# Performance work log

Hardware: AMD Instinct MI355X
Metric: run time of the kernel (lower is better)

Reference implementation:

```python
import jax, jax.numpy as jnp
import numpy as np

N = 50000      # nodes
E = 800000     # edges
R = 8          # relations
DIN, DH, DOUT = 128, 128, 64
EPS = 1e-5     # BatchNorm eps


def setup_inputs() -> dict:
    key = jax.random.key(0)
    ks = jax.random.split(key, 24)
    w = lambda k, shape, fan_in: jax.random.normal(k, shape, jnp.float32) / np.sqrt(fan_in)
    x = jax.random.normal(ks[0], (N, DIN), jnp.float32)
    edge_index = jax.random.randint(ks[1], (2, E), 0, N, dtype=jnp.int64)
    edge_type = jax.random.randint(ks[2], (E,), 0, R, dtype=jnp.int64)
    return {
        "x": x, "edge_index": edge_index, "edge_type": edge_type,
        # layer 1: RGCN(DIN->DH) + BN
        "W1": w(ks[3], (R, DIN, DH), DIN), "Wr1": w(ks[4], (DIN, DH), DIN), "b1": jnp.zeros((DH,), jnp.float32),
        "g1": jnp.ones((DH,), jnp.float32), "be1": jnp.zeros((DH,), jnp.float32),
        "rm1": 0.1 * jax.random.normal(ks[5], (DH,), jnp.float32),
        "rv1": jax.random.uniform(ks[6], (DH,), jnp.float32, 0.5, 1.5),
        # layer 2: RGCN(DH->DH) + BN
        "W2": w(ks[7], (R, DH, DH), DH), "Wr2": w(ks[8], (DH, DH), DH), "b2": jnp.zeros((DH,), jnp.float32),
        "g2": jnp.ones((DH,), jnp.float32), "be2": jnp.zeros((DH,), jnp.float32),
        "rm2": 0.1 * jax.random.normal(ks[9], (DH,), jnp.float32),
        "rv2": jax.random.uniform(ks[10], (DH,), jnp.float32, 0.5, 1.5),
        # layer 3: RGCN(DH->DOUT)
        "W3": w(ks[11], (R, DH, DOUT), DH), "Wr3": w(ks[12], (DH, DOUT), DH), "b3": jnp.zeros((DOUT,), jnp.float32),
    }


def rgcn_layer(x, W, Wroot, b, src, dst, et):
    # PyG RGCNConv: per-relation linear transform, per-relation MEAN aggregation
    # over incoming edges, plus root transform and bias.
    nR, nN, H = W.shape[0], x.shape[0], W.shape[2]
    h = jnp.einsum('nd,rdh->rnh', x, W)          # [R,N,H] per-relation transform
    msg = h[et, src]                             # [E,H] gather per edge
    seg = dst * nR + et                          # segment key = (node, relation)
    sums = jax.ops.segment_sum(msg, seg, num_segments=nN * nR)
    cnt = jax.ops.segment_sum(jnp.ones((seg.shape[0],), x.dtype), seg, num_segments=nN * nR)
    mean = sums / jnp.maximum(cnt, 1.0)[:, None]
    agg = mean.reshape(nN, nR, H).sum(axis=1)    # sum over relations
    return agg + x @ Wroot + b


def batchnorm(x, g, b, rm, rv):
    # eval-mode BatchNorm1d with running stats
    return (x - rm) * jax.lax.rsqrt(rv + EPS) * g + b


def reference(x, edge_index, edge_type,
              W1, Wr1, b1, g1, be1, rm1, rv1,
              W2, Wr2, b2, g2, be2, rm2, rv2,
              W3, Wr3, b3):
    src, dst = edge_index[0], edge_index[1]
    h = rgcn_layer(x, W1, Wr1, b1, src, dst, edge_type)
    h = jax.nn.relu(batchnorm(h, g1, be1, rm1, rv1))  # dropout: eval mode = identity
    h = rgcn_layer(h, W2, Wr2, b2, src, dst, edge_type)
    h = jax.nn.relu(batchnorm(h, g2, be2, rm2, rv2))
    h = rgcn_layer(h, W3, Wr3, b3, src, dst, edge_type)
    return jax.nn.sigmoid(h)
```

## Files before the change

kernel.cpp:

```cpp
#include <hip/hip_runtime.h>

typedef _Float16 f16;
typedef __attribute__((ext_vector_type(8))) _Float16 half8;
typedef __attribute__((ext_vector_type(2))) _Float16 half2v;
typedef __attribute__((ext_vector_type(4))) float float4v;

#define NNODES 50000
#define NEDGES 800000
#define NREL 8
#define NRSEG (NNODES * NREL)
#define KDIM 1152
#define CAP 16
#define CAPQ (CAP / 4)
#define NT64 ((NNODES + 63) / 64)

__global__ void bucket_fill(const int* __restrict__ src, const int* __restrict__ dst,
                            const int* __restrict__ et, int* __restrict__ cnt,
                            int* __restrict__ esrc) {
    int e = blockIdx.x * blockDim.x + threadIdx.x;
    if (e < NEDGES) {
        int s = dst[e] * NREL + et[e];
        int p = atomicAdd(&cnt[s], 1);
        if (p < CAP) esrc[s * CAP + p] = src[e];
    }
}

__global__ void setup_misc(const float* __restrict__ x, f16* __restrict__ x16,
                           const float* __restrict__ W1, const float* __restrict__ Wr1,
                           const float* __restrict__ W2, const float* __restrict__ Wr2,
                           const float* __restrict__ W3, const float* __restrict__ Wr3,
                           f16* __restrict__ Bt, int* __restrict__ cnt) {
    int t = blockIdx.x * blockDim.x + threadIdx.x;
    if (t < NNODES * 64) {
        float2 v = ((const float2*)x)[t];
        half2v o = {(f16)v.x, (f16)v.y};
        ((half2v*)x16)[t] = o;
        return;
    }
    int idx = t - NNODES * 64;
    if (idx < 320 * KDIM) {
        int hg = idx / KDIM, k = idx - hg * KDIM;
        const float *W, *Wr;
        int h, H;
        if (hg < 128)      { W = W1; Wr = Wr1; h = hg;       H = 128; }
        else if (hg < 256) { W = W2; Wr = Wr2; h = hg - 128; H = 128; }
        else               { W = W3; Wr = Wr3; h = hg - 256; H = 64;  }
        float v = (k < 1024) ? W[(size_t)k * H + h] : Wr[(size_t)(k - 1024) * H + h];
        Bt[idx] = (f16)v;
        return;
    }
    int z = idx - 320 * KDIM;
    if (z < NRSEG / 4) ((int4*)cnt)[z] = (int4){0, 0, 0, 0};
}

template <int H, int HB, int MODE>
__global__ __launch_bounds__(256, 4) void fused_layer(
    const f16* __restrict__ act, const f16* __restrict__ Bt,
    const int* __restrict__ cnt, const int* __restrict__ esrc,
    const float* __restrict__ bias, const float* __restrict__ g,
    const float* __restrict__ be, const float* __restrict__ rm,
    const float* __restrict__ rv, f16* __restrict__ hout, float* __restrict__ fout) {
    constexpr int NT = HB / 16;
    __shared__ f16 Ws[HB][128];
    const int tid = threadIdx.x;
    const int wave = tid >> 6, lane = tid & 63;
    const int l15 = lane & 15, quad = lane >> 4;
    const int m0 = blockIdx.x * 64 + wave * 16;
    const int nh = blockIdx.y;
    int node = m0 + l15;
    node = node < NNODES ? node : NNODES - 1;

    int4 cq0 = ((const int4*)cnt)[node * 2];
    int4 cq1 = ((const int4*)cnt)[node * 2 + 1];
    int cnts[8] = {cq0.x, cq0.y, cq0.z, cq0.w, cq1.x, cq1.y, cq1.z, cq1.w};
    const int4* bq_base = (const int4*)esrc + (size_t)node * NREL * CAPQ;

    float4v acc[NT];
#pragma unroll
    for (int j = 0; j < NT; ++j) acc[j] = (float4v){0.f, 0.f, 0.f, 0.f};

    int4 qp0 = bq_base[0];
    int4 qp1 = bq_base[CAPQ];

#pragma unroll
    for (int r = 0; r < 9; ++r) {
        __syncthreads();
#pragma unroll
        for (int i = 0; i < NT; ++i) {
            int G = i * 256 + tid;
            int row = G >> 4, gg = G & 15;
            half8 v = *(const half8*)(Bt + (size_t)(nh * HB + row) * KDIM +
                                      r * 128 + gg * 8);
            *(half8*)&Ws[row][((gg ^ (row & 7))) * 8] = v;
        }
        half8 ch[4];
#pragma unroll
        for (int t = 0; t < 4; ++t) ch[t] = (half8)(f16)0.f;
        if (r < 8) {
            int truelen = cnts[r];
            int len = truelen < CAP ? truelen : CAP;
            f16 invh = (f16)(truelen > 1 ? 1.f / (float)truelen : 1.f);
            const int4* bq = bq_base + r * CAPQ;
            int4 q0 = qp0;
            qp0 = qp1;
            if (r < 6) qp1 = bq_base[(r + 2) * CAPQ];
            for (int j4 = 0; j4 < (len + 3) >> 2; ++j4) {
                int4 q = (j4 == 0) ? q0 : bq[j4];
                int ids[4] = {q.x, q.y, q.z, q.w};
                int base = j4 * 4;
#pragma unroll
                for (int t = 0; t < 4; ++t) {
                    if (base + t < len) {
                        const half8* rp = (const half8*)(act + (size_t)ids[t] * 128 + quad * 8);
                        half8 v0 = rp[0], v1 = rp[4], v2 = rp[8], v3 = rp[12];
                        ch[0] += v0;
                        ch[1] += v1;
                        ch[2] += v2;
                        ch[3] += v3;
                    }
                }
            }
            half8 sv;
#pragma unroll
            for (int u = 0; u < 8; ++u) sv[u] = invh;
#pragma unroll
            for (int t = 0; t < 4; ++t) ch[t] *= sv;
        } else {
#pragma unroll
            for (int ks = 0; ks < 4; ++ks)
                ch[ks] = *(const half8*)(act + (size_t)node * 128 + ks * 32 + quad * 8);
        }
        __syncthreads();
#pragma unroll
        for (int ks = 0; ks < 4; ++ks) {
#pragma unroll
            for (int nt = 0; nt < NT; ++nt) {
                int row = nt * 16 + l15;
                half8 bf = *(const half8*)&Ws[row][(((ks * 4 + quad) ^ (row & 7))) * 8];
                acc[nt] = __builtin_amdgcn_mfma_f32_16x16x32_f16(ch[ks], bf, acc[nt], 0, 0, 0);
            }
        }
    }

#pragma unroll
    for (int nt = 0; nt < NT; ++nt) {
        int col = nh * HB + nt * 16 + l15;
        float alpha, beta;
        if (MODE == 0) {
            float sc = g[col] * rsqrtf(rv[col] + 1e-5f);
            alpha = sc;
            beta = (bias[col] - rm[col]) * sc + be[col];
        } else {
            alpha = 1.f;
            beta = bias[col];
        }
#pragma unroll
        for (int rg = 0; rg < 4; ++rg) {
            int row = m0 + quad * 4 + rg;
            if (row < NNODES) {
                float v = fmaf(acc[nt][rg], alpha, beta);
                if (MODE == 0) {
                    hout[(size_t)row * H + col] = (f16)fmaxf(v, 0.f);
                } else {
                    fout[(size_t)row * H + col] = 1.f / (1.f + __expf(-v));
                }
            }
        }
    }
}

extern "C" void kernel_launch(void* const* d_in, const int* in_sizes, int n_in,
                              void* d_out, int out_size, void* d_ws, size_t ws_size,
                              hipStream_t stream) {
    (void)in_sizes; (void)n_in; (void)out_size; (void)ws_size;
    const float* x   = (const float*)d_in[0];
    const int* ei    = (const int*)d_in[1];
    const int* et    = (const int*)d_in[2];
    const float* W1  = (const float*)d_in[3];
    const float* Wr1 = (const float*)d_in[4];
    const float* b1  = (const float*)d_in[5];
    const float* g1  = (const float*)d_in[6];
    const float* be1 = (const float*)d_in[7];
    const float* rm1 = (const float*)d_in[8];
    const float* rv1 = (const float*)d_in[9];
    const float* W2  = (const float*)d_in[10];
    const float* Wr2 = (const float*)d_in[11];
    const float* b2  = (const float*)d_in[12];
    const float* g2  = (const float*)d_in[13];
    const float* be2 = (const float*)d_in[14];
    const float* rm2 = (const float*)d_in[15];
    const float* rv2 = (const float*)d_in[16];
    const float* W3  = (const float*)d_in[17];
    const float* Wr3 = (const float*)d_in[18];
    const float* b3  = (const float*)d_in[19];
    const int* src = ei;
    const int* dst = ei + NEDGES;
    float* out = (float*)d_out;

    char* ws = (char*)d_ws;
    size_t off = 0;
    auto alloc = [&](size_t bytes) -> void* {
        off = (off + 255) & ~(size_t)255;
        void* p = ws + off;
        off += bytes;
        return p;
    };
    int* cnt  = (int*)alloc((size_t)NRSEG * 4);
    int* esrc = (int*)alloc((size_t)NRSEG * CAP * 4);
    f16* x16  = (f16*)alloc((size_t)NNODES * 128 * 2);
    f16* ha   = (f16*)alloc((size_t)NNODES * 128 * 2);
    f16* hb   = (f16*)alloc((size_t)NNODES * 128 * 2);
    f16* Bt   = (f16*)alloc((size_t)320 * KDIM * 2);

    const int SETUP_T = NNODES * 64 + 320 * KDIM + NRSEG / 4;
    setup_misc<<<(SETUP_T + 255) / 256, 256, 0, stream>>>(
        x, x16, W1, Wr1, W2, Wr2, W3, Wr3, Bt, cnt);
    bucket_fill<<<(NEDGES + 255) / 256, 256, 0, stream>>>(src, dst, et, cnt, esrc);

    fused_layer<128, 64, 0><<<dim3(NT64, 2), 256, 0, stream>>>(x16, Bt, cnt, esrc,
                                                               b1, g1, be1, rm1, rv1, ha, nullptr);
    fused_layer<128, 64, 0><<<dim3(NT64, 2), 256, 0, stream>>>(ha, Bt + (size_t)128 * KDIM, cnt, esrc,
                                                               b2, g2, be2, rm2, rv2, hb, nullptr);
    fused_layer<64, 32, 1><<<dim3(NT64, 2), 256, 0, stream>>>(hb, Bt + (size_t)256 * KDIM, cnt, esrc,
                                                              b3, nullptr, nullptr, nullptr, nullptr,
                                                              nullptr, out);
}
```

Baseline: 464.1 us.

## Sort per-segment source buckets and compute full output width per block

Adds a bucket_sort kernel that sorts each (node, relation) bucket of source indices, so the later gathers read neighbour rows in ascending address order and get better cache locality. The fused layers now launch one block per 64-node tile covering the whole output width instead of splitting it across two blocks, which removes the duplicated gather and aggregation work. The costs are an extra kernel launch with a sort pass over all 400K segments, and heavier per-block work that may raise register pressure and cut occupancy.

```diff
diff --git a/kernel.cpp b/kernel.cpp
--- a/kernel.cpp
+++ b/kernel.cpp
@@ -13,6 +13,7 @@
 #define CAP 16
 #define CAPQ (CAP / 4)
 #define NT64 ((NNODES + 63) / 64)
+#define IMAX 0x7fffffff
 
 __global__ void bucket_fill(const int* __restrict__ src, const int* __restrict__ dst,
                             const int* __restrict__ et, int* __restrict__ cnt,
@@ -22,6 +23,48 @@
         int s = dst[e] * NREL + et[e];
         int p = atomicAdd(&cnt[s], 1);
         if (p < CAP) esrc[s * CAP + p] = src[e];
+    }
+}
+
+__device__ __forceinline__ void ce(int& a, int& b) {
+    int lo = min(a, b), hi = max(a, b);
+    a = lo; b = hi;
+}
+__global__ void bucket_sort(const int* __restrict__ cnt, int* __restrict__ esrc) {
+    int s = blockIdx.x * blockDim.x + threadIdx.x;
+    if (s >= NRSEG) return;
+    int len = cnt[s];
+    len = len < CAP ? len : CAP;
+    if (len < 2) return;
+    int* b = esrc + (size_t)s * CAP;
+    if (len <= 4) {
+        int4 q = *(int4*)b;
+        int v0 = q.x, v1 = len > 1 ? q.y : IMAX;
+        int v2 = len > 2 ? q.z : IMAX, v3 = len > 3 ? q.w : IMAX;
+        ce(v0, v1); ce(v2, v3); ce(v0, v2); ce(v1, v3); ce(v1, v2);
+        *(int4*)b = (int4){v0, v1, v2, v3};
+    } else if (len <= 8) {
+        int4 qa = ((int4*)b)[0], qb = ((int4*)b)[1];
+        int v0 = qa.x, v1 = qa.y, v2 = qa.z, v3 = qa.w;
+        int v4 = qb.x, v5 = len > 5 ? qb.y : IMAX;
+        int v6 = len > 6 ? qb.z : IMAX, v7 = len > 7 ? qb.w : IMAX;
+        ce(v0, v1); ce(v2, v3); ce(v4, v5); ce(v6, v7);
+        ce(v0, v2); ce(v1, v3); ce(v4, v6); ce(v5, v7);
+        ce(v1, v2); ce(v5, v6);
+        ce(v0, v4); ce(v1, v5); ce(v2, v6); ce(v3, v7);
+        ce(v2, v4); ce(v3, v5);
+        ce(v1, v2); ce(v3, v4); ce(v5, v6);
+        ((int4*)b)[0] = (int4){v0, v1, v2, v3};
+        ((int4*)b)[1] = (int4){v4, v5, v6, v7};
+    } else {
+        int v[CAP];
+        for (int i = 0; i < len; ++i) v[i] = b[i];
+        for (int i = 1; i < len; ++i) {
+            int key = v[i], j = i - 1;
+            while (j >= 0 && v[j] > key) { v[j + 1] = v[j]; --j; }
+            v[j + 1] = key;
+        }
+        for (int i = 0; i < len; ++i) b[i] = v[i];
     }
 }
 
@@ -216,12 +259,13 @@
     setup_misc<<<(SETUP_T + 255) / 256, 256, 0, stream>>>(
         x, x16, W1, Wr1, W2, Wr2, W3, Wr3, Bt, cnt);
     bucket_fill<<<(NEDGES + 255) / 256, 256, 0, stream>>>(src, dst, et, cnt, esrc);
-
-    fused_layer<128, 64, 0><<<dim3(NT64, 2), 256, 0, stream>>>(x16, Bt, cnt, esrc,
-                                                               b1, g1, be1, rm1, rv1, ha, nullptr);
-    fused_layer<128, 64, 0><<<dim3(NT64, 2), 256, 0, stream>>>(ha, Bt + (size_t)128 * KDIM, cnt, esrc,
-                                                               b2, g2, be2, rm2, rv2, hb, nullptr);
-    fused_layer<64, 32, 1><<<dim3(NT64, 2), 256, 0, stream>>>(hb, Bt + (size_t)256 * KDIM, cnt, esrc,
+    bucket_sort<<<(NRSEG + 255) / 256, 256, 0, stream>>>(cnt, esrc);
+
+    fused_layer<128, 128, 0><<<dim3(NT64, 1), 256, 0, stream>>>(x16, Bt, cnt, esrc,
+                                                                b1, g1, be1, rm1, rv1, ha, nullptr);
+    fused_layer<128, 128, 0><<<dim3(NT64, 1), 256, 0, stream>>>(ha, Bt + (size_t)128 * KDIM, cnt, esrc,
+                                                                b2, g2, be2, rm2, rv2, hb, nullptr);
+    fused_layer<64, 64, 1><<<dim3(NT64, 1), 256, 0, stream>>>(hb, Bt + (size_t)256 * KDIM, cnt, esrc,
                                                               b3, nullptr, nullptr, nullptr, nullptr,
                                                               nullptr, out);
 }
```

Measured after the change: 374.5 us. 1.24x faster.
